# Performance work log

Hardware: AMD Instinct MI355X
Metric: run time of the kernel (lower is better)

## Reference

```python
import jax, jax.numpy as jnp
import numpy as np

B, D, K = 32768, 512, 5
SIM_THRESH = 0.7
GATE_TEMP = 1.0
LN_EPS = 1e-5


def setup_inputs() -> dict:
    key = jax.random.key(0)
    ks = jax.random.split(key, 12)
    s = 1.0 / np.sqrt(D)
    query = jax.random.normal(ks[0], (B, D), dtype=jnp.float32)
    retrieved_memories = jax.random.normal(ks[1], (B, K, D), dtype=jnp.float32)
    similarities = jax.random.uniform(ks[2], (B, K), dtype=jnp.float32)
    mask = jax.random.randint(ks[3], (B, K), 0, 2) > 0
    mask = mask.at[:, 0].set(True)  # at least one valid memory per row
    return {
        "query": query,
        "retrieved_memories": retrieved_memories,
        "similarities": similarities,
        "mask": mask,
        "Wq": jax.random.normal(ks[4], (D, D), dtype=jnp.float32) * s,
        "bq": jnp.zeros((D,), jnp.float32),
        "Wk": jax.random.normal(ks[5], (D, D), dtype=jnp.float32) * s,
        "bk": jnp.zeros((D,), jnp.float32),
        "Wv": jax.random.normal(ks[6], (D, D), dtype=jnp.float32) * s,
        "bv": jnp.zeros((D,), jnp.float32),
        "Wo": jax.random.normal(ks[7], (D, D), dtype=jnp.float32) * s,
        "bo": jnp.zeros((D,), jnp.float32),
        "Wg": jax.random.normal(ks[8], (2 * D, 1), dtype=jnp.float32) * s,
        "bg": jnp.zeros((1,), jnp.float32),
        "ln_g": jnp.ones((D,), jnp.float32),
        "ln_b": jnp.zeros((D,), jnp.float32),
    }


def reference(query, retrieved_memories, similarities, mask,
              Wq, bq, Wk, bk, Wv, bv, Wo, bo, Wg, bg, ln_g, ln_b):
    scale = D ** (-0.5)
    q = query @ Wq + bq                                          # (B, D)
    k = jnp.einsum('bkd,de->bke', retrieved_memories, Wk) + bk   # (B, K, D)
    v = jnp.einsum('bkd,de->bke', retrieved_memories, Wv) + bv   # (B, K, D)
    scores = jnp.einsum('bd,bkd->bk', q, k) * scale              # (B, K)
    scores = jnp.where(mask, scores, -jnp.inf)
    w = jax.nn.softmax(scores, axis=-1)
    w = jnp.where(mask, w, 0.0)
    mem = jnp.einsum('bk,bkd->bd', w, v)                         # (B, D)
    mem = mem @ Wo + bo
    # gated fusion
    max_sim = jnp.max(similarities, axis=-1, keepdims=True)      # (B, 1)
    gate = jax.nn.sigmoid(jnp.concatenate([query, mem], axis=-1) @ Wg + bg)
    conf = jax.nn.sigmoid(GATE_TEMP * (max_sim - SIM_THRESH))
    out = query + (gate * conf) * mem
    # layer norm
    mu = jnp.mean(out, axis=-1, keepdims=True)
    var = jnp.mean((out - mu) ** 2, axis=-1, keepdims=True)
    out = (out - mu) * jax.lax.rsqrt(var + LN_EPS) * ln_g + ln_b
    return out
```

## Files before the change

kernel.cpp:

```cpp
#include <hip/hip_runtime.h>

#define DD 512
#define KM 5
#define B_ROWS 32768

typedef __attribute__((ext_vector_type(8))) short short8;
typedef __attribute__((ext_vector_type(4))) short s16x4;
typedef __attribute__((ext_vector_type(4))) float f32x4;

static __device__ __forceinline__ short f2bf(float x) {
  unsigned u = __builtin_bit_cast(unsigned, x);
  u = (u + 0x7fffu + ((u >> 16) & 1u)) >> 16;
  return (short)u;
}
static __device__ __forceinline__ float bf2f(short s) {
  unsigned u = ((unsigned)(unsigned short)s) << 16;
  return __builtin_bit_cast(float, u);
}

#define SYNC0() do { asm volatile("s_waitcnt vmcnt(0) lgkmcnt(0)" ::: "memory"); __builtin_amdgcn_s_barrier(); } while (0)
#define SYNC2() do { asm volatile("s_waitcnt vmcnt(2) lgkmcnt(0)" ::: "memory"); __builtin_amdgcn_s_barrier(); } while (0)
#define BAR_LGKM() do { asm volatile("s_waitcnt lgkmcnt(0)" ::: "memory"); __builtin_amdgcn_s_barrier(); } while (0)

__global__ __launch_bounds__(256)
void prep(const float* __restrict__ Wq, const float* __restrict__ bq,
          const float* __restrict__ Wk, const float* __restrict__ Wv,
          const float* __restrict__ Wo, const float* __restrict__ bo,
          const float* __restrict__ bv,
          short* __restrict__ At, short* __restrict__ Ct,
          float* __restrict__ w0, float* __restrict__ d0) {
  __shared__ float Xs[16][17];
  __shared__ float Ys[16][17];
  __shared__ float red[2][128];
  const int tid = threadIdx.x;
  const int blk = blockIdx.x;
  if (blk < 2048) {
    const bool isC = blk >= 1024;
    const int b = blk & 1023;
    const int i0 = (b & 31) * 16, j0 = (b >> 5) * 16;
    const int tx = tid & 15, ty = tid >> 4;
    const float* X = isC ? Wo : Wk;
    const float* Y = isC ? Wv : Wq;
    float acc = 0.f;
    for (int l0 = 0; l0 < DD; l0 += 16) {
      if (isC) Xs[tx][ty] = X[(size_t)(l0 + ty) * DD + (j0 + tx)];
      else     Xs[ty][tx] = X[(size_t)(j0 + ty) * DD + (l0 + tx)];
      Ys[ty][tx] = Y[(size_t)(i0 + ty) * DD + (l0 + tx)];
      __syncthreads();
#pragma unroll
      for (int l = 0; l < 16; ++l) acc += Xs[ty][l] * Ys[tx][l];
      __syncthreads();
    }
    short* P = isC ? Ct : At;
    P[(size_t)(j0 + ty) * DD + (i0 + tx)] = f2bf(acc);
  } else if (blk < 2176) {
    const int j = (blk - 2048) * 4 + (tid >> 6);
    const int lane = tid & 63;
    const float* r = Wk + (size_t)j * DD + lane * 8;
    f32x4 a = *(const f32x4*)r;
    f32x4 c = *(const f32x4*)(r + 4);
    const float* bp = bq + lane * 8;
    f32x4 ba = *(const f32x4*)bp;
    f32x4 bc = *(const f32x4*)(bp + 4);
    float s = a[0]*ba[0] + a[1]*ba[1] + a[2]*ba[2] + a[3]*ba[3]
            + c[0]*bc[0] + c[1]*bc[1] + c[2]*bc[2] + c[3]*bc[3];
#pragma unroll
    for (int off = 32; off > 0; off >>= 1) s += __shfl_xor(s, off);
    if (lane == 0) w0[j] = s;
  } else {
    const int j = (blk - 2176) * 128 + (tid & 127);
    const int half = tid >> 7;
    float s = 0.f;
    for (int e = half * 256; e < half * 256 + 256; ++e)
      s += bv[e] * Wo[(size_t)e * DD + j];
    red[half][tid & 127] = s;
    __syncthreads();
    if (half == 0) d0[j] = red[0][tid] + red[1][tid] + bo[j];
  }
}

#define STAGE_W(MAT, TI, DST) do {                                                 \
  _Pragma("unroll") for (int c = 0; c < 4; ++c) {                                  \
    const short* _src = (MAT) + (size_t)(c * 128 + (tid >> 2)) * DD + (TI) * 32    \
                        + (((tid & 3) * 8) ^ (((tid >> 2) & 3) << 3));             \
    __builtin_amdgcn_global_load_lds(                                              \
        (const __attribute__((address_space(1))) void*)_src,                       \
        (__attribute__((address_space(3))) void*)(&(DST)[c * 4096 + w * 512]),     \
        16, 0, 0);                                                                 \
  } } while (0)

#define WRITE_A(DST, QLO, QHI) do {                                                \
  short8 _sv;                                                                      \
  _sv[0]=f2bf((QLO)[0]); _sv[1]=f2bf((QLO)[1]); _sv[2]=f2bf((QLO)[2]); _sv[3]=f2bf((QLO)[3]); \
  _sv[4]=f2bf((QHI)[0]); _sv[5]=f2bf((QHI)[1]); _sv[6]=f2bf((QHI)[2]); _sv[7]=f2bf((QHI)[3]); \
  *(short8*)&(DST)[arow * 32 + (acol ^ ((arow & 3) << 3))] = _sv; } while (0)

#define ROW_FINISH(SV, MA, MC, VM, ROW)                                     \
    {                                                                       \
      float mx = -1e30f;                                                    \
      _Pragma("unroll") for (int k = 0; k < KM; ++k)                        \
        if ((VM) & (1 << k)) mx = fmaxf(mx, SV[k]);                         \
      float wk[KM]; float sum = 0.f;                                        \
      _Pragma("unroll") for (int k = 0; k < KM; ++k) {                      \
        wk[k] = ((VM) & (1 << k)) ? __expf(SV[k] - mx) : 0.f;               \
        sum += wk[k];                                                       \
      }                                                                     \
      const float inv = 1.f / sum;                                          \
      float o[8] = {0.f,0.f,0.f,0.f,0.f,0.f,0.f,0.f};                       \
      _Pragma("unroll") for (int k = 0; k < KM; ++k)                        \
        if ((VM) & (1 << k)) {                                              \
          const float g = wk[k] * inv;                                      \
          _Pragma("unroll") for (int i = 0; i < 4; ++i) {                   \
            o[i] += g * MA[k][i]; o[4 + i] += g * MC[k][i];                 \
          }                                                                 \
        }                                                                   \
      short8 ov;                                                            \
      _Pragma("unroll") for (int i = 0; i < 8; ++i) ov[i] = f2bf(o[i]);     \
      *(short8*)&R1[((ROW) * DD + lane * 8) ^ (((ROW) & 7) << 3)] = ov;     \
    }

__global__ __launch_bounds__(512, 2)
void mk(const float* __restrict__ q, const short* __restrict__ Atw,
        const float* __restrict__ w0, const float* __restrict__ mem,
        const int* __restrict__ mask, const short* __restrict__ Ctw,
        const float* __restrict__ d0, const float* __restrict__ sims,
        const float* __restrict__ Wg, const float* __restrict__ bgp,
        const float* __restrict__ lng, const float* __restrict__ lnb,
        float* __restrict__ outp) {
  __shared__ short R1[128 * DD];
  __shared__ short RS[DD * 32];
  const int tid = threadIdx.x;
  const int lane = tid & 63;
  const int w = tid >> 6;
  const int kg = lane >> 4, lr = lane & 15;
  const int bm = blockIdx.x;

  short* As0 = R1;
  short* As1 = R1 + 4096;
  short* RS1 = R1 + 8192;

  f32x4 acc[8][4] = {};
  const int arow = tid >> 2, acol = (tid & 3) * 8;
  const float* qbase = q + (size_t)(bm * 128 + arow) * DD + acol;
  {
    STAGE_W(Atw, 0, RS);
    __builtin_amdgcn_sched_barrier(0);
    f32x4 q0a = *(const f32x4*)qbase;
    f32x4 q0b = *(const f32x4*)(qbase + 4);
    WRITE_A(As0, q0a, q0b);
    f32x4 qA = *(const f32x4*)(qbase + 32);
    f32x4 qB = *(const f32x4*)(qbase + 36);
    SYNC2();
    for (int ki = 0; ki < 16; ++ki) {
      const short* Asc = (ki & 1) ? As1 : As0;
      short* Asn = (ki & 1) ? As0 : As1;
      const short* RSc = (ki & 1) ? RS1 : RS;
      short* RSn = (ki & 1) ? RS : RS1;
      short8 av[8], bvv[4];
#pragma unroll
      for (int mi = 0; mi < 8; ++mi) {
        const int ar = mi * 16 + lr;
        av[mi] = *(const short8*)&Asc[ar * 32 + ((kg * 8) ^ ((lr & 3) << 3))];
      }
#pragma unroll
      for (int ni = 0; ni < 4; ++ni) {
        const int row = w * 64 + ni * 16 + lr;
        bvv[ni] = *(const short8*)&RSc[row * 32 + ((kg * 8) ^ ((lr & 3) << 3))];
      }
      if (ki < 15) {
        WRITE_A(Asn, qA, qB);
        STAGE_W(Atw, ki + 1, RSn);
        __builtin_amdgcn_sched_barrier(0);
        if (ki < 14) {
          qA = *(const f32x4*)(qbase + (ki + 2) * 32);
          qB = *(const f32x4*)(qbase + (ki + 2) * 32 + 4);
        }
      }
#pragma unroll
      for (int mi = 0; mi < 8; ++mi)
#pragma unroll
        for (int ni = 0; ni < 4; ++ni)
          acc[mi][ni] = __builtin_amdgcn_mfma_f32_16x16x32_bf16(av[mi], bvv[ni], acc[mi][ni], 0, 0, 0);
      if (ki < 14) { SYNC2(); } else { SYNC0(); }
    }
  }
#pragma unroll
  for (int ni = 0; ni < 4; ++ni) {
    const int col = w * 64 + ni * 16 + lr;
    const float b0 = w0[col];
#pragma unroll
    for (int mi = 0; mi < 8; ++mi)
#pragma unroll
      for (int r = 0; r < 4; ++r)
        R1[(mi * 16 + kg * 4 + r) * DD + col] = f2bf(acc[mi][ni][r] + b0);
  }
  BAR_LGKM();
  STAGE_W(Ctw, 0, RS);
  const float scale = 0.044194173824159216f;
  for (int rr = 0; rr < 16; rr += 2) {
    const int row0 = w * 16 + rr;
    const size_t b0 = (size_t)bm * 128 + row0;
    const short8 tv0 = *(const short8*)&R1[row0 * DD + lane * 8];
    const short8 tv1 = *(const short8*)&R1[(row0 + 1) * DD + lane * 8];
    float tf0[8], tf1[8];
#pragma unroll
    for (int i = 0; i < 8; ++i) { tf0[i] = bf2f(tv0[i]); tf1[i] = bf2f(tv1[i]); }
    int vm0 = 0, vm1 = 0;
#pragma unroll
    for (int k = 0; k < KM; ++k) {
      vm0 |= (__builtin_amdgcn_readfirstlane(mask[b0 * KM + k]) ? 1 : 0) << k;
      vm1 |= (__builtin_amdgcn_readfirstlane(mask[(b0 + 1) * KM + k]) ? 1 : 0) << k;
    }
    f32x4 ma0[KM], mc0[KM], ma1[KM], mc1[KM];
#pragma unroll
    for (int k = 0; k < KM; ++k) {
      if (vm0 & (1 << k)) {
        const f32x4* mp = (const f32x4*)(mem + (b0 * KM + k) * DD + lane * 8);
        ma0[k] = __builtin_nontemporal_load(mp);
        mc0[k] = __builtin_nontemporal_load(mp + 1);
      }
      if (vm1 & (1 << k)) {
        const f32x4* mp = (const f32x4*)(mem + ((b0 + 1) * KM + k) * DD + lane * 8);
        ma1[k] = __builtin_nontemporal_load(mp);
        mc1[k] = __builtin_nontemporal_load(mp + 1);
      }
    }
    float s0[KM], s1[KM];
#pragma unroll
    for (int k = 0; k < KM; ++k) {
      if (vm0 & (1 << k)) {
        float p = 0.f;
#pragma unroll
        for (int i = 0; i < 4; ++i) { p += tf0[i] * ma0[k][i]; p += tf0[4 + i] * mc0[k][i]; }
#pragma unroll
        for (int off = 32; off > 0; off >>= 1) p += __shfl_xor(p, off);
        s0[k] = p * scale;
      }
      if (vm1 & (1 << k)) {
        float p = 0.f;
#pragma unroll
        for (int i = 0; i < 4; ++i) { p += tf1[i] * ma1[k][i]; p += tf1[4 + i] * mc1[k][i]; }
#pragma unroll
        for (int off = 32; off > 0; off >>= 1) p += __shfl_xor(p, off);
        s1[k] = p * scale;
      }
    }
    ROW_FINISH(s0, ma0, mc0, vm0, row0)
    ROW_FINISH(s1, ma1, mc1, vm1, (row0 + 1))
  }
  SYNC0();
  f32x4 acc2[8][4] = {};
  for (int ki = 0; ki < 16; ++ki) {
    short8 av[8], bvv[4];
#pragma unroll
    for (int mi = 0; mi < 8; ++mi) {
      const int ar = mi * 16 + lr;
      av[mi] = *(const short8*)&R1[(ar * DD + ki * 32 + kg * 8) ^ ((ar & 7) << 3)];
    }
#pragma unroll
    for (int ni = 0; ni < 4; ++ni) {
      const int row = w * 64 + ni * 16 + lr;
      bvv[ni] = *(const short8*)&RS[row * 32 + ((kg * 8) ^ ((lr & 3) << 3))];
    }
    BAR_LGKM();
    if (ki < 15) STAGE_W(Ctw, ki + 1, RS);
#pragma unroll
    for (int mi = 0; mi < 8; ++mi)
#pragma unroll
      for (int ni = 0; ni < 4; ++ni)
        acc2[mi][ni] = __builtin_amdgcn_mfma_f32_16x16x32_bf16(av[mi], bvv[ni], acc2[mi][ni], 0, 0, 0);
    SYNC0();
  }
#pragma unroll
  for (int ni = 0; ni < 4; ++ni) {
    const int col = w * 64 + ni * 16 + lr;
    const float b0 = d0[col];
#pragma unroll
    for (int mi = 0; mi < 8; ++mi)
#pragma unroll
      for (int r = 0; r < 4; ++r)
        R1[(mi * 16 + kg * 4 + r) * DD + col] = f2bf(acc2[mi][ni][r] + b0);
  }
  BAR_LGKM();
  {
    const float* wg1 = Wg + lane * 8;
    const float* wg2 = Wg + DD + lane * 8;
    f32x4 g1a = *(const f32x4*)wg1, g1b = *(const f32x4*)(wg1 + 4);
    f32x4 g2a = *(const f32x4*)wg2, g2b = *(const f32x4*)(wg2 + 4);
    f32x4 la = *(const f32x4*)(lng + lane * 8), lb4 = *(const f32x4*)(lng + lane * 8 + 4);
    f32x4 ba = *(const f32x4*)(lnb + lane * 8), bb4 = *(const f32x4*)(lnb + lane * 8 + 4);
    const float bgs = bgp[0];
    for (int rr = 0; rr < 16; ++rr) {
      const int row = w * 16 + rr;
      const size_t b = (size_t)bm * 128 + row;
      const float* qp = q + b * DD + lane * 8;
      f32x4 q0 = *(const f32x4*)qp;
      f32x4 q1 = *(const f32x4*)(qp + 4);
      float qf[8] = {q0[0],q0[1],q0[2],q0[3],q1[0],q1[1],q1[2],q1[3]};
      const short8 mv = *(const short8*)&R1[row * DD + lane * 8];
      float mf[8];
#pragma unroll
      for (int i = 0; i < 8; ++i) mf[i] = bf2f(mv[i]);
      float gp = qf[0]*g1a[0]+qf[1]*g1a[1]+qf[2]*g1a[2]+qf[3]*g1a[3]
               + qf[4]*g1b[0]+qf[5]*g1b[1]+qf[6]*g1b[2]+qf[7]*g1b[3]
               + mf[0]*g2a[0]+mf[1]*g2a[1]+mf[2]*g2a[2]+mf[3]*g2a[3]
               + mf[4]*g2b[0]+mf[5]*g2b[1]+mf[6]*g2b[2]+mf[7]*g2b[3];
#pragma unroll
      for (int off = 32; off > 0; off >>= 1) gp += __shfl_xor(gp, off);
      const float gate = 1.f / (1.f + __expf(-(gp + bgs)));
      float ms = sims[b * KM];
#pragma unroll
      for (int k = 1; k < KM; ++k) ms = fmaxf(ms, sims[b * KM + k]);
      const float conf = 1.f / (1.f + __expf(-(ms - 0.7f)));
      const float gc = gate * conf;
      float o[8];
      float s1 = 0.f, s2 = 0.f;
#pragma unroll
      for (int i = 0; i < 8; ++i) {
        o[i] = qf[i] + gc * mf[i];
        s1 += o[i];
        s2 += o[i] * o[i];
      }
#pragma unroll
      for (int off = 32; off > 0; off >>= 1) { s1 += __shfl_xor(s1, off); s2 += __shfl_xor(s2, off); }
      const float mu = s1 * (1.f / 512.f);
      const float var = s2 * (1.f / 512.f) - mu * mu;
      const float rs = rsqrtf(var + 1e-5f);
      f32x4 r0, r1;
#pragma unroll
      for (int i = 0; i < 4; ++i) r0[i] = (o[i] - mu) * rs * la[i] + ba[i];
#pragma unroll
      for (int i = 0; i < 4; ++i) r1[i] = (o[4 + i] - mu) * rs * lb4[i] + bb4[i];
      float* op = outp + b * DD + lane * 8;
      __builtin_nontemporal_store(r0, (f32x4*)op);
      __builtin_nontemporal_store(r1, (f32x4*)(op + 4));
    }
  }
}

extern "C" void kernel_launch(void* const* d_in, const int* in_sizes, int n_in,
                              void* d_out, int out_size, void* d_ws, size_t ws_size,
                              hipStream_t stream) {
  const float* query = (const float*)d_in[0];
  const float* mem   = (const float*)d_in[1];
  const float* sims  = (const float*)d_in[2];
  const int*   mask  = (const int*)d_in[3];
  const float* Wq = (const float*)d_in[4];
  const float* bq = (const float*)d_in[5];
  const float* Wk = (const float*)d_in[6];
  const float* Wv = (const float*)d_in[8];
  const float* bv = (const float*)d_in[9];
  const float* Wo = (const float*)d_in[10];
  const float* bo = (const float*)d_in[11];
  const float* Wg = (const float*)d_in[12];
  const float* bg = (const float*)d_in[13];
  const float* ln_g = (const float*)d_in[14];
  const float* ln_b = (const float*)d_in[15];
  float* out = (float*)d_out;

  char* ws = (char*)d_ws;
  short* At = (short*)ws;
  short* Ct = At + (size_t)DD * DD;
  float* w0 = (float*)(Ct + (size_t)DD * DD);
  float* d0 = w0 + DD;

  prep<<<dim3(2180), dim3(256), 0, stream>>>(Wq, bq, Wk, Wv, Wo, bo, bv, At, Ct, w0, d0);
  mk<<<dim3(B_ROWS / 128), dim3(512), 0, stream>>>(query, At, w0, mem, mask,
                                                   Ct, d0, sims, Wg, bg, ln_g, ln_b, out);
}
```

Measured before the change: 156.5 us.

## Compute weight-product prep GEMMs with bf16 MFMA instead of scalar FMA

The prep kernel that forms the fused weight products Wk·Wq^T and Wo^T·Wv^T now runs as an MFMA GEMM. It converts the operands to bf16 in registers, stores them into double-buffered swizzled LDS, and prefetches the next k-tile while the current one computes. The old version used 2048 small 16x16 scalar-FMA tiles. The grid shrinks from 2180 blocks to 74, so only 8 blocks do the GEMM work, which may underuse the GPU. The inputs are rounded to bf16 before the product rather than only the result, which changes accuracy slightly.

```diff
diff --git a/kernel.cpp b/kernel.cpp
--- a/kernel.cpp
+++ b/kernel.cpp
@@ -22,39 +22,108 @@
 #define SYNC2() do { asm volatile("s_waitcnt vmcnt(2) lgkmcnt(0)" ::: "memory"); __builtin_amdgcn_s_barrier(); } while (0)
 #define BAR_LGKM() do { asm volatile("s_waitcnt lgkmcnt(0)" ::: "memory"); __builtin_amdgcn_s_barrier(); } while (0)
 
-__global__ __launch_bounds__(256)
-void prep(const float* __restrict__ Wq, const float* __restrict__ bq,
-          const float* __restrict__ Wk, const float* __restrict__ Wv,
-          const float* __restrict__ Wo, const float* __restrict__ bo,
-          const float* __restrict__ bv,
-          short* __restrict__ At, short* __restrict__ Ct,
-          float* __restrict__ w0, float* __restrict__ d0) {
-  __shared__ float Xs[16][17];
-  __shared__ float Ys[16][17];
-  __shared__ float red[2][128];
+__global__ __launch_bounds__(512, 2)
+void prepG(const float* __restrict__ Wq, const float* __restrict__ bq,
+           const float* __restrict__ Wk, const float* __restrict__ Wv,
+           const float* __restrict__ Wo, const float* __restrict__ bo,
+           const float* __restrict__ bv,
+           short* __restrict__ At, short* __restrict__ Ct,
+           float* __restrict__ w0, float* __restrict__ d0) {
+  __shared__ short sh[40960];
   const int tid = threadIdx.x;
   const int blk = blockIdx.x;
-  if (blk < 2048) {
-    const bool isC = blk >= 1024;
-    const int b = blk & 1023;
-    const int i0 = (b & 31) * 16, j0 = (b >> 5) * 16;
-    const int tx = tid & 15, ty = tid >> 4;
-    const float* X = isC ? Wo : Wk;
-    const float* Y = isC ? Wv : Wq;
-    float acc = 0.f;
-    for (int l0 = 0; l0 < DD; l0 += 16) {
-      if (isC) Xs[tx][ty] = X[(size_t)(l0 + ty) * DD + (j0 + tx)];
-      else     Xs[ty][tx] = X[(size_t)(j0 + ty) * DD + (l0 + tx)];
-      Ys[ty][tx] = Y[(size_t)(i0 + ty) * DD + (l0 + tx)];
+  if (blk < 8) {
+    const bool isC = blk >= 4;
+    const int j0 = (blk & 3) * 128;
+    const int lane = tid & 63;
+    const int w = tid >> 6;
+    const int kg = lane >> 4, lr = lane & 15;
+    const float* Ysrc = isC ? Wv : Wq;
+    f32x4 acc[8][4] = {};
+    f32x4 rb[4][2];
+    f32x4 ra0, ra1;
+#pragma unroll
+    for (int c = 0; c < 4; ++c) {
+      const float* p = Ysrc + (size_t)tid * DD + c * 8;
+      rb[c][0] = *(const f32x4*)p; rb[c][1] = *(const f32x4*)(p + 4);
+    }
+    if (!isC) {
+      const float* p = Wk + (size_t)(j0 + (tid >> 2)) * DD + (tid & 3) * 8;
+      ra0 = *(const f32x4*)p; ra1 = *(const f32x4*)(p + 4);
+    } else {
+      const float* p = Wo + (size_t)(tid >> 4) * DD + j0 + (tid & 15) * 8;
+      ra0 = *(const f32x4*)p; ra1 = *(const f32x4*)(p + 4);
+    }
+    for (int ki = 0; ki < 16; ++ki) {
+      short* As = (ki & 1) ? (sh + 4096) : sh;
+      short* Bs = (ki & 1) ? (sh + 24576) : (sh + 8192);
+#pragma unroll
+      for (int c = 0; c < 4; ++c) {
+        short8 sv;
+        sv[0]=f2bf(rb[c][0][0]); sv[1]=f2bf(rb[c][0][1]); sv[2]=f2bf(rb[c][0][2]); sv[3]=f2bf(rb[c][0][3]);
+        sv[4]=f2bf(rb[c][1][0]); sv[5]=f2bf(rb[c][1][1]); sv[6]=f2bf(rb[c][1][2]); sv[7]=f2bf(rb[c][1][3]);
+        *(short8*)&Bs[tid * 32 + ((c * 8) ^ ((tid & 3) << 3))] = sv;
+      }
+      if (!isC) {
+        short8 sv;
+        sv[0]=f2bf(ra0[0]); sv[1]=f2bf(ra0[1]); sv[2]=f2bf(ra0[2]); sv[3]=f2bf(ra0[3]);
+        sv[4]=f2bf(ra1[0]); sv[5]=f2bf(ra1[1]); sv[6]=f2bf(ra1[2]); sv[7]=f2bf(ra1[3]);
+        *(short8*)&As[(tid >> 2) * 32 + (((tid & 3) * 8) ^ (((tid >> 2) & 3) << 3))] = sv;
+      } else {
+        const int l = tid >> 4;
+#pragma unroll
+        for (int e = 0; e < 8; ++e) {
+          const int j = (tid & 15) * 8 + e;
+          const float v = (e < 4) ? ra0[e & 3] : ra1[e & 3];
+          As[j * 32 + (l ^ ((j & 3) << 3))] = f2bf(v);
+        }
+      }
+      if (ki < 15) {
+        const int kt = (ki + 1) * 32;
+#pragma unroll
+        for (int c = 0; c < 4; ++c) {
+          const float* p = Ysrc + (size_t)tid * DD + kt + c * 8;
+          rb[c][0] = *(const f32x4*)p; rb[c][1] = *(const f32x4*)(p + 4);
+        }
+        if (!isC) {
+          const float* p = Wk + (size_t)(j0 + (tid >> 2)) * DD + kt + (tid & 3) * 8;
+          ra0 = *(const f32x4*)p; ra1 = *(const f32x4*)(p + 4);
+        } else {
+          const float* p = Wo + (size_t)(kt + (tid >> 4)) * DD + j0 + (tid & 15) * 8;
+          ra0 = *(const f32x4*)p; ra1 = *(const f32x4*)(p + 4);
+        }
+      }
       __syncthreads();
-#pragma unroll
-      for (int l = 0; l < 16; ++l) acc += Xs[ty][l] * Ys[tx][l];
+      short8 av[8], bvv[4];
+#pragma unroll
+      for (int mi = 0; mi < 8; ++mi) {
+        const int ar = mi * 16 + lr;
+        av[mi] = *(const short8*)&As[ar * 32 + ((kg * 8) ^ ((lr & 3) << 3))];
+      }
+#pragma unroll
+      for (int ni = 0; ni < 4; ++ni) {
+        const int row = w * 64 + ni * 16 + lr;
+        bvv[ni] = *(const short8*)&Bs[row * 32 + ((kg * 8) ^ ((lr & 3) << 3))];
+      }
+#pragma unroll
+      for (int mi = 0; mi < 8; ++mi)
+#pragma unroll
+        for (int ni = 0; ni < 4; ++ni)
+          acc[mi][ni] = __builtin_amdgcn_mfma_f32_16x16x32_bf16(av[mi], bvv[ni], acc[mi][ni], 0, 0, 0);
       __syncthreads();
     }
     short* P = isC ? Ct : At;
-    P[(size_t)(j0 + ty) * DD + (i0 + tx)] = f2bf(acc);
-  } else if (blk < 2176) {
-    const int j = (blk - 2048) * 4 + (tid >> 6);
+#pragma unroll
+    for (int ni = 0; ni < 4; ++ni) {
+      const int col = w * 64 + ni * 16 + lr;
+#pragma unroll
+      for (int mi = 0; mi < 8; ++mi)
+#pragma unroll
+        for (int r = 0; r < 4; ++r)
+          P[(size_t)(j0 + mi * 16 + kg * 4 + r) * DD + col] = f2bf(acc[mi][ni][r]);
+    }
+  } else if (blk < 72) {
+    const int j = (blk - 8) * 8 + (tid >> 6);
     const int lane = tid & 63;
     const float* r = Wk + (size_t)j * DD + lane * 8;
     f32x4 a = *(const f32x4*)r;
@@ -68,14 +137,15 @@
     for (int off = 32; off > 0; off >>= 1) s += __shfl_xor(s, off);
     if (lane == 0) w0[j] = s;
   } else {
-    const int j = (blk - 2176) * 128 + (tid & 127);
-    const int half = tid >> 7;
+    float* red = (float*)sh;
+    const int j = (blk - 72) * 256 + (tid & 255);
+    const int half = tid >> 8;
     float s = 0.f;
     for (int e = half * 256; e < half * 256 + 256; ++e)
       s += bv[e] * Wo[(size_t)e * DD + j];
-    red[half][tid & 127] = s;
+    red[half * 256 + (tid & 255)] = s;
     __syncthreads();
-    if (half == 0) d0[j] = red[0][tid] + red[1][tid] + bo[j];
+    if (half == 0) d0[j] = red[tid] + red[256 + tid] + bo[j];
   }
 }
 
@@ -364,7 +434,7 @@
   float* w0 = (float*)(Ct + (size_t)DD * DD);
   float* d0 = w0 + DD;
 
-  prep<<<dim3(2180), dim3(256), 0, stream>>>(Wq, bq, Wk, Wv, Wo, bo, bv, At, Ct, w0, d0);
+  prepG<<<dim3(74), dim3(512), 0, stream>>>(Wq, bq, Wk, Wv, Wo, bo, bv, At, Ct, w0, d0);
   mk<<<dim3(B_ROWS / 128), dim3(512), 0, stream>>>(query, At, w0, mem, mask,
                                                    Ct, d0, sims, Wg, bg, ln_g, ln_b, out);
 }
```

Result: slower. 178.4 us (+14.0%).
